# Optimization experiments

Hardware: AMD Instinct MI355X
Metric: run time of the kernel (lower is better)

The kernel has to match this reference:

```python
import jax, jax.numpy as jnp
import numpy as np

B, T, K = 16, 8, 4          # batch, num task vectors, num param blocks
DIN, H1, F, MH = 9408, 1024, 512, 128  # encoder dims; MetaNet hidden


def _pool(x):
    # 4x4 average pool then flatten: [B,3,224,224] -> [B, 3*56*56]
    b = x.shape[0]
    return x.reshape(b, 3, 56, 4, 56, 4).mean(axis=(3, 5)).reshape(b, -1)


def setup_inputs() -> dict:
    key = jax.random.key(0)
    ks = jax.random.split(key, 13)
    n = lambda k, shp, sc: jax.random.normal(k, shp, jnp.float32) * sc
    return {
        "x": jax.random.normal(ks[0], (B, 3, 224, 224), jnp.float32),
        "W1": n(ks[1], (DIN, H1), 0.02), "b1": n(ks[2], (H1,), 0.02),
        "W2": n(ks[3], (H1, F), 0.02),  "b2": n(ks[4], (F,), 0.02),
        "dW1": n(ks[5], (T, DIN, H1), 0.01), "db1": n(ks[6], (T, H1), 0.01),
        "dW2": n(ks[7], (T, H1, F), 0.01),   "db2": n(ks[8], (T, F), 0.01),
        # MetaNet: Linear(F,MH) init std=0.01, ReLU, Linear(MH, T*K)
        "mW1": n(ks[9], (F, MH), 0.01), "mb1": n(ks[10], (MH,), 0.01),
        "mW2": n(ks[11], (MH, T * K), 0.02), "mb2": n(ks[12], (T * K,), 0.02),
    }


def reference(x, W1, b1, W2, b2, dW1, db1, dW2, db2, mW1, mb1, mW2, mb2):
    xp = _pool(x)  # [B, DIN]
    # base features with frozen base params (torch.no_grad)
    base = jax.lax.stop_gradient(
        jax.nn.relu(xp @ W1 + b1) @ W2 + b2)  # [B, F]
    # MetaNet -> blockwise coefficients [B, T, K]; block order (W1,b1,W2,b2)
    coefs = (jax.nn.relu(base @ mW1 + mb1) @ mW2 + mb2).reshape(B, T, K)
    cW1, cb1, cW2, cb2 = coefs[:, :, 0], coefs[:, :, 1], coefs[:, :, 2], coefs[:, :, 3]
    # per-sample composed forward; (W1 + sum_t c*dW1) applied to xp, factored
    # so the [B,DIN,H1] composed weight is never materialized:
    h_tv = jnp.einsum("bi,tij->btj", xp, dW1)            # [B,T,H1]
    h = jax.nn.relu(xp @ W1 + jnp.einsum("bt,btj->bj", cW1, h_tv)
                    + b1 + jnp.einsum("bt,tj->bj", cb1, db1))  # [B,H1]
    o_tv = jnp.einsum("bj,tjk->btk", h, dW2)             # [B,T,F]
    out = (h @ W2 + jnp.einsum("bt,btk->bk", cW2, o_tv)
           + b2 + jnp.einsum("bt,tk->bk", cb2, db2))     # [B,F]
    return out
```

## Files before the change

kernel.cpp:

```cpp
#include <hip/hip_runtime.h>
#include <cstdint>
#include <cstddef>


typedef float f2_t __attribute__((ext_vector_type(2)));
typedef float f4_t __attribute__((ext_vector_type(4)));

__global__ void pool_kernel(const float* __restrict__ x, float* __restrict__ xp) {
  int idx = blockIdx.x * 256 + threadIdx.x;
  int bc = idx / 3136;
  int r  = idx - bc * 3136;
  int i  = r / 56;
  int j  = r - i * 56;
  const float* src = x + ((size_t)bc * 224 + 4 * i) * 224 + 4 * j;
  float s = 0.f;
#pragma unroll
  for (int rr = 0; rr < 4; ++rr) {
    float4 v = *reinterpret_cast<const float4*>(src + rr * 224);
    s += v.x + v.y + v.z + v.w;
  }
  xp[idx] = s * 0.0625f;
}

template<int KC, int VEC, int UF, int NT>
__device__ __forceinline__ void gemm_pipe(
    const float* a_s, int row0, const float* Brow, int N, float (&acc)[16][VEC])
{
  static_assert(KC % UF == 0, "");
  constexpr int NG = KC / UF;
  static_assert(NG >= 2, "");
  float w0[UF][VEC], w1[UF][VEC];

  auto loadg = [&](float (&W)[UF][VEC], int kb) {
#pragma unroll
    for (int u = 0; u < UF; ++u) {
      const float* p = Brow + (size_t)(kb + u) * N;
      if constexpr (VEC == 2) {
        f2_t v;
        if constexpr (NT) v = __builtin_nontemporal_load(reinterpret_cast<const f2_t*>(p));
        else              v = *reinterpret_cast<const f2_t*>(p);
        W[u][0] = v.x; W[u][1] = v.y;
      } else {
        f4_t v;
        if constexpr (NT) v = __builtin_nontemporal_load(reinterpret_cast<const f4_t*>(p));
        else              v = *reinterpret_cast<const f4_t*>(p);
        W[u][0] = v.x; W[u][1] = v.y; W[u][2] = v.z; W[u][3] = v.w;
      }
    }
  };
  auto comp = [&](const float (&W)[UF][VEC], int kb) {
#pragma unroll
    for (int u = 0; u < UF; ++u) {
      int kk = row0 + kb + u;
      const float4 a0 = *reinterpret_cast<const float4*>(&a_s[kk * 20 + 0]);
      const float4 a1 = *reinterpret_cast<const float4*>(&a_s[kk * 20 + 4]);
      const float4 a2 = *reinterpret_cast<const float4*>(&a_s[kk * 20 + 8]);
      const float4 a3 = *reinterpret_cast<const float4*>(&a_s[kk * 20 + 12]);
      const float av[16] = {a0.x, a0.y, a0.z, a0.w, a1.x, a1.y, a1.z, a1.w,
                            a2.x, a2.y, a2.z, a2.w, a3.x, a3.y, a3.z, a3.w};
#pragma unroll
      for (int b = 0; b < 16; ++b)
#pragma unroll
        for (int v = 0; v < VEC; ++v)
          acc[b][v] = fmaf(av[b], W[u][v], acc[b][v]);
    }
  };

  loadg(w0, 0);
  if constexpr (NG % 2 == 0) {
#pragma unroll 1
    for (int g = 0; g + 2 < NG; g += 2) {
      loadg(w1, (g + 1) * UF);
      comp(w0, g * UF);
      loadg(w0, (g + 2) * UF);
      comp(w1, (g + 1) * UF);
    }
    loadg(w1, (NG - 1) * UF);
    comp(w0, (NG - 2) * UF);
    comp(w1, (NG - 1) * UF);
  } else {
#pragma unroll 1
    for (int g = 0; g + 3 < NG; g += 2) {
      loadg(w1, (g + 1) * UF);
      comp(w0, g * UF);
      loadg(w0, (g + 2) * UF);
      comp(w1, (g + 1) * UF);
    }
    loadg(w1, (NG - 2) * UF);
    comp(w0, (NG - 3) * UF);
    loadg(w0, (NG - 1) * UF);
    comp(w1, (NG - 2) * UF);
    comp(w0, (NG - 1) * UF);
  }
}

template<int KC, int VEC, int UF, int NT, int BS>
__global__ __launch_bounds__(BS) void skinny_gemm(
    const float* __restrict__ A, int ldA,
    const float* __restrict__ B,
    const float* __restrict__ A2, int ldA2,
    const float* __restrict__ B2,
    int chunkSplit, int chunksPerT,
    const float* __restrict__ coefs4,
    int N, float* __restrict__ P)
{
  __shared__ float a_s[KC * 20];
  const int c = blockIdx.x, tid = threadIdx.x;

  const float* Ab;
  const float* Bb;
  int lda, iLoc0, t = 0;
  bool scaled = false;
  if (c < chunkSplit) {
    Ab = A; lda = ldA;
    if (chunksPerT > 0) {
      t = c / chunksPerT;
      iLoc0 = (c - t * chunksPerT) * KC;
    } else {
      iLoc0 = c * KC;
    }
    scaled = (coefs4 != nullptr);
    Bb = B + (size_t)c * KC * N;
  } else {
    Ab = A2; lda = ldA2;
    iLoc0 = (c - chunkSplit) * KC;
    Bb = B2 + (size_t)iLoc0 * N;
  }

  for (int b = 0; b < 16; ++b) {
    float s = scaled ? coefs4[b * 32 + t * 4] : 1.f;
    const float* Arow = Ab + (size_t)b * lda + iLoc0;
    for (int kk = tid; kk < KC; kk += BS)
      a_s[kk * 20 + b] = s * Arow[kk];
  }
  __syncthreads();

  const int j0 = (blockIdx.y * BS + tid) * VEC;
  float acc[16][VEC];
#pragma unroll
  for (int b = 0; b < 16; ++b)
#pragma unroll
    for (int v = 0; v < VEC; ++v) acc[b][v] = 0.f;

  gemm_pipe<KC, VEC, UF, NT>(a_s, 0, Bb + j0, N, acc);

  float* Pb = P + (size_t)c * 16 * N + j0;
#pragma unroll
  for (int b = 0; b < 16; ++b) {
    if constexpr (VEC == 2) {
      f2_t v = {acc[b][0], acc[b][1]};
      __builtin_nontemporal_store(v, reinterpret_cast<f2_t*>(Pb));
    } else {
      f4_t v = {acc[b][0], acc[b][1], acc[b][2], acc[b][3]};
      __builtin_nontemporal_store(v, reinterpret_cast<f4_t*>(Pb));
    }
    Pb += N;
  }
}

__global__ __launch_bounds__(512, 2) void gbig_kernel(
    const float* __restrict__ xp,
    const float* __restrict__ W1,
    const float* __restrict__ dW1,
    float* __restrict__ P1, float* __restrict__ P3)
{
  __shared__ float a_s[294 * 20];
  __shared__ float lds2[256 * 65];
  const int tid = threadIdx.x;

  if (blockIdx.x < 224) {
    const int c = blockIdx.x;
    for (int b = 0; b < 16; ++b) {
      const float* Arow = xp + (size_t)b * 9408 + c * 42;
      for (int kk = tid; kk < 42; kk += 512) a_s[kk * 20 + b] = Arow[kk];
    }
    __syncthreads();

    const int j0 = tid * 2;
    float acc[16][2];
#pragma unroll
    for (int b = 0; b < 16; ++b) { acc[b][0] = 0.f; acc[b][1] = 0.f; }
    gemm_pipe<42, 2, 7, 1>(a_s, 0, W1 + (size_t)c * 42 * 1024 + j0, 1024, acc);

    float* Pb = P1 + (size_t)c * 16 * 1024 + j0;
#pragma unroll
    for (int b = 0; b < 16; ++b) {
      f2_t v = {acc[b][0], acc[b][1]};
      __builtin_nontemporal_store(v, reinterpret_cast<f2_t*>(Pb));
      Pb += 1024;
    }
  } else {
    const int c = blockIdx.x - 224;
    const int t = c >> 5, il = (c & 31) * 294;
    for (int b = 0; b < 16; ++b) {
      const float* Arow = xp + (size_t)b * 9408 + il;
      for (int kk = tid; kk < 294; kk += 512) a_s[kk * 20 + b] = Arow[kk];
    }
    __syncthreads();

    const int half = tid >> 8, t256 = tid & 255;
    const int j0 = t256 * 4;
    float acc[16][4];
#pragma unroll
    for (int b = 0; b < 16; ++b)
#pragma unroll
      for (int v = 0; v < 4; ++v) acc[b][v] = 0.f;

    gemm_pipe<147, 4, 7, 1>(a_s, half * 147,
                            dW1 + ((size_t)t * 9408 + il + half * 147) * 1024 + j0,
                            1024, acc);

    if (half) {
      float* dst = &lds2[t256 * 65];
#pragma unroll
      for (int b = 0; b < 16; ++b)
#pragma unroll
        for (int v = 0; v < 4; ++v) dst[b * 4 + v] = acc[b][v];
    }
    __syncthreads();
    if (!half) {
      const float* src = &lds2[t256 * 65];
      float* Pb = P3 + (size_t)c * 16 * 1024 + j0;
#pragma unroll
      for (int b = 0; b < 16; ++b) {
        f4_t v = {acc[b][0] + src[b * 4 + 0], acc[b][1] + src[b * 4 + 1],
                  acc[b][2] + src[b * 4 + 2], acc[b][3] + src[b * 4 + 3]};
        __builtin_nontemporal_store(v, reinterpret_cast<f4_t*>(Pb));
        Pb += 1024;
      }
    }
  }
}

template<int NCH, int MODE, int FTOT>
__global__ __launch_bounds__(256) void reduce4(
    const float* __restrict__ P,
    const float* __restrict__ bias,
    const float* __restrict__ coefs,
    const float* __restrict__ dvec,
    float* __restrict__ o1, float* __restrict__ o2)
{
  constexpr int CPS = NCH / 16;
  static_assert(NCH % 16 == 0, "");
  __shared__ float4 r[16][17];
  const int fl = threadIdx.x & 15, s = threadIdx.x >> 4;
  const int f = blockIdx.x * 64 + fl * 4;

  const f4_t* p = reinterpret_cast<const f4_t*>(P + (size_t)s * CPS * FTOT + f);
  float sx = 0.f, sy = 0.f, sz = 0.f, sw = 0.f;
#pragma unroll 8
  for (int cc = 0; cc < CPS; ++cc) {
    f4_t v = __builtin_nontemporal_load(p);
    sx += v.x; sy += v.y; sz += v.z; sw += v.w;
    p += FTOT / 4;
  }
  if constexpr (MODE == 3) {
    int b = f >> 10;
    float sc = coefs[b * 32 + (s >> 1) * 4];
    sx *= sc; sy *= sc; sz *= sc; sw *= sc;
  }
  r[s][fl] = make_float4(sx, sy, sz, sw);
  __syncthreads();

  if (s == 0) {
    float vx = 0.f, vy = 0.f, vz = 0.f, vw = 0.f;
#pragma unroll
    for (int i = 0; i < 16; ++i) {
      float4 t = r[i][fl];
      vx += t.x; vy += t.y; vz += t.z; vw += t.w;
    }
    if constexpr (MODE == 1) {
      float4 bb = *reinterpret_cast<const float4*>(bias + (f & 1023));
      float4 z = make_float4(vx + bb.x, vy + bb.y, vz + bb.z, vw + bb.w);
      *reinterpret_cast<float4*>(o1 + f) = z;
      *reinterpret_cast<float4*>(o2 + f) =
          make_float4(fmaxf(z.x, 0.f), fmaxf(z.y, 0.f), fmaxf(z.z, 0.f), fmaxf(z.w, 0.f));
    } else if constexpr (MODE == 3) {
      int b = f >> 10, j = f & 1023;
      float4 zz = *reinterpret_cast<const float4*>(bias + f);
      float zx = vx + zz.x, zy = vy + zz.y, zzc = vz + zz.z, zw = vw + zz.w;
#pragma unroll
      for (int t = 0; t < 8; ++t) {
        float c1 = coefs[b * 32 + t * 4 + 1];
        float4 d = *reinterpret_cast<const float4*>(dvec + t * 1024 + j);
        zx = fmaf(c1, d.x, zx); zy = fmaf(c1, d.y, zy);
        zzc = fmaf(c1, d.z, zzc); zw = fmaf(c1, d.w, zw);
      }
      *reinterpret_cast<float4*>(o1 + f) =
          make_float4(fmaxf(zx, 0.f), fmaxf(zy, 0.f), fmaxf(zzc, 0.f), fmaxf(zw, 0.f));
    } else {
      int b = f >> 9, k = f & 511;
      float4 bb = *reinterpret_cast<const float4*>(bias + k);
      float zx = vx + bb.x, zy = vy + bb.y, zzc = vz + bb.z, zw = vw + bb.w;
#pragma unroll
      for (int t = 0; t < 8; ++t) {
        float c3 = coefs[b * 32 + t * 4 + 3];
        float4 d = *reinterpret_cast<const float4*>(dvec + t * 512 + k);
        zx = fmaf(c3, d.x, zx); zy = fmaf(c3, d.y, zy);
        zzc = fmaf(c3, d.z, zzc); zw = fmaf(c3, d.w, zw);
      }
      *reinterpret_cast<float4*>(o1 + f) = make_float4(zx, zy, zzc, zw);
    }
  }
}

__global__ __launch_bounds__(512) void tail2_kernel(
    const float* __restrict__ P2, const float* __restrict__ b2,
    const float* __restrict__ mW1, const float* __restrict__ mb1,
    const float* __restrict__ mW2, const float* __restrict__ mb2,
    float* __restrict__ coefs)
{
  __shared__ float bs[512];
  __shared__ float pm[4][129];
  __shared__ float ms[128];
  __shared__ float p3[16][33];
  const int b = blockIdx.x, tid = threadIdx.x;

  float s = b2[tid];
  const float* p = P2 + b * 512 + tid;
#pragma unroll 8
  for (int c = 0; c < 128; ++c) { s += *p; p += 8192; }
  bs[tid] = s;
  __syncthreads();

  {
    int col = tid & 127, kq = tid >> 7;
    const float* br = &bs[kq * 128];
    const float* w = mW1 + (size_t)(kq * 128) * 128 + col;
    float m0 = 0.f, m1 = 0.f, m2 = 0.f, m3 = 0.f;
    for (int k = 0; k < 128; k += 4) {
      m0 = fmaf(br[k + 0], w[(k + 0) * 128], m0);
      m1 = fmaf(br[k + 1], w[(k + 1) * 128], m1);
      m2 = fmaf(br[k + 2], w[(k + 2) * 128], m2);
      m3 = fmaf(br[k + 3], w[(k + 3) * 128], m3);
    }
    pm[kq][col] = (m0 + m1) + (m2 + m3);
  }
  __syncthreads();
  if (tid < 128)
    ms[tid] = fmaxf(mb1[tid] + (pm[0][tid] + pm[1][tid]) + (pm[2][tid] + pm[3][tid]), 0.f);
  __syncthreads();

  {
    int o = tid & 31, kq = tid >> 5;
    float a = 0.f;
#pragma unroll
    for (int kk = 0; kk < 8; ++kk)
      a = fmaf(ms[kq * 8 + kk], mW2[(kq * 8 + kk) * 32 + o], a);
    p3[kq][o] = a;
  }
  __syncthreads();
  if (tid < 32) {
    float a = mb2[tid];
#pragma unroll
    for (int q = 0; q < 16; ++q) a += p3[q][tid];
    coefs[b * 32 + tid] = a;
  }
}

extern "C" void kernel_launch(void* const* d_in, const int* in_sizes, int n_in,
                              void* d_out, int out_size, void* d_ws, size_t ws_size,
                              hipStream_t stream) {
  const float* x   = (const float*)d_in[0];
  const float* W1  = (const float*)d_in[1];
  const float* b1  = (const float*)d_in[2];
  const float* W2  = (const float*)d_in[3];
  const float* b2  = (const float*)d_in[4];
  const float* dW1 = (const float*)d_in[5];
  const float* db1 = (const float*)d_in[6];
  const float* dW2 = (const float*)d_in[7];
  const float* db2 = (const float*)d_in[8];
  const float* mW1 = (const float*)d_in[9];
  const float* mb1 = (const float*)d_in[10];
  const float* mW2 = (const float*)d_in[11];
  const float* mb2 = (const float*)d_in[12];
  float* out = (float*)d_out;

  float* ws    = (float*)d_ws;
  float* xp    = ws;
  float* z1    = xp + 150528;
  float* t1    = z1 + 16384;
  float* coefs = t1 + 16384;
  float* h     = coefs + 512;
  float* P1    = h + 16384;
  float* P2    = P1 + 3670016;
  float* P3    = P2 + 1048576;
  float* P4    = P3 + 4194304;

  const int BIG = 1 << 30;

  pool_kernel<<<588, 256, 0, stream>>>(x, xp);

  gbig_kernel<<<480, 512, 0, stream>>>(xp, W1, dW1, P1, P3);

  reduce4<224, 1, 16384><<<256, 256, 0, stream>>>(P1, b1, nullptr, nullptr, z1, t1);

  skinny_gemm<8, 2, 4, 0, 256><<<dim3(128, 1), 256, 0, stream>>>(
      t1, 1024, W2, nullptr, 0, nullptr, BIG, 0, nullptr, 512, P2);

  tail2_kernel<<<16, 512, 0, stream>>>(P2, b2, mW1, mb1, mW2, mb2, coefs);

  reduce4<256, 3, 16384><<<256, 256, 0, stream>>>(P3, z1, coefs, db1, h, nullptr);

  skinny_gemm<32, 2, 8, 1, 256><<<dim3(288, 1), 256, 0, stream>>>(
      h, 1024, dW2, h, 1024, W2, 256, 32, coefs + 2, 512, P4);

  reduce4<288, 4, 8192><<<128, 256, 0, stream>>>(P4, b2, coefs, db2, out, nullptr);
}
```

Baseline: 133.3 us.

## Fuse pooling into big GEMM and merge W1 reduction with W2 GEMM

```diff
diff --git a/kernel.cpp b/kernel.cpp
--- a/kernel.cpp
+++ b/kernel.cpp
@@ -5,22 +5,6 @@
 
 typedef float f2_t __attribute__((ext_vector_type(2)));
 typedef float f4_t __attribute__((ext_vector_type(4)));
-
-__global__ void pool_kernel(const float* __restrict__ x, float* __restrict__ xp) {
-  int idx = blockIdx.x * 256 + threadIdx.x;
-  int bc = idx / 3136;
-  int r  = idx - bc * 3136;
-  int i  = r / 56;
-  int j  = r - i * 56;
-  const float* src = x + ((size_t)bc * 224 + 4 * i) * 224 + 4 * j;
-  float s = 0.f;
-#pragma unroll
-  for (int rr = 0; rr < 4; ++rr) {
-    float4 v = *reinterpret_cast<const float4*>(src + rr * 224);
-    s += v.x + v.y + v.z + v.w;
-  }
-  xp[idx] = s * 0.0625f;
-}
 
 template<int KC, int VEC, int UF, int NT>
 __device__ __forceinline__ void gemm_pipe(
@@ -94,6 +78,145 @@
   }
 }
 
+template<int KC, int NTHR>
+__device__ __forceinline__ void stage_pool(float* a_s, const float* __restrict__ x, int il) {
+  for (int idx = threadIdx.x; idx < 16 * KC; idx += NTHR) {
+    int b = idx / KC, kk = idx - b * KC;
+    int i = il + kk;
+    int ch = i / 3136, r = i - ch * 3136;
+    int pi = r / 56, pj = r - pi * 56;
+    const float* src = x + ((size_t)(b * 3 + ch) * 224 + 4 * pi) * 224 + 4 * pj;
+    float4 v0 = *reinterpret_cast<const float4*>(src);
+    float4 v1 = *reinterpret_cast<const float4*>(src + 224);
+    float4 v2 = *reinterpret_cast<const float4*>(src + 448);
+    float4 v3 = *reinterpret_cast<const float4*>(src + 672);
+    float s = (v0.x + v0.y + v0.z + v0.w) + (v1.x + v1.y + v1.z + v1.w)
+            + (v2.x + v2.y + v2.z + v2.w) + (v3.x + v3.y + v3.z + v3.w);
+    a_s[kk * 20 + b] = s * 0.0625f;
+  }
+}
+
+__global__ __launch_bounds__(512, 2) void gbig_kernel(
+    const float* __restrict__ x,
+    const float* __restrict__ W1,
+    const float* __restrict__ dW1,
+    float* __restrict__ P1, float* __restrict__ P3)
+{
+  __shared__ float a_s[294 * 20];
+  __shared__ float lds2[256 * 65];
+  const int tid = threadIdx.x;
+
+  if (blockIdx.x < 112) {
+    const int c = blockIdx.x;
+    stage_pool<84, 512>(a_s, x, c * 84);
+    __syncthreads();
+
+    const int j0 = tid * 2;
+    float acc[16][2];
+#pragma unroll
+    for (int b = 0; b < 16; ++b) { acc[b][0] = 0.f; acc[b][1] = 0.f; }
+    gemm_pipe<84, 2, 7, 1>(a_s, 0, W1 + (size_t)c * 84 * 1024 + j0, 1024, acc);
+
+    float* Pb = P1 + (size_t)c * 16 * 1024 + j0;
+#pragma unroll
+    for (int b = 0; b < 16; ++b) {
+      f2_t v = {acc[b][0], acc[b][1]};
+      __builtin_nontemporal_store(v, reinterpret_cast<f2_t*>(Pb));
+      Pb += 1024;
+    }
+  } else {
+    const int c = blockIdx.x - 112;
+    const int t = c >> 5, il = (c & 31) * 294;
+    stage_pool<294, 512>(a_s, x, il);
+    __syncthreads();
+
+    const int half = tid >> 8, t256 = tid & 255;
+    const int j0 = t256 * 4;
+    float acc[16][4];
+#pragma unroll
+    for (int b = 0; b < 16; ++b)
+#pragma unroll
+      for (int v = 0; v < 4; ++v) acc[b][v] = 0.f;
+
+    gemm_pipe<147, 4, 7, 1>(a_s, half * 147,
+                            dW1 + ((size_t)t * 9408 + il + half * 147) * 1024 + j0,
+                            1024, acc);
+
+    if (half) {
+      float* dst = &lds2[t256 * 65];
+#pragma unroll
+      for (int b = 0; b < 16; ++b)
+#pragma unroll
+        for (int v = 0; v < 4; ++v) dst[b * 4 + v] = acc[b][v];
+    }
+    __syncthreads();
+    if (!half) {
+      const float* src = &lds2[t256 * 65];
+      float* Pb = P3 + (size_t)c * 16 * 1024 + j0;
+#pragma unroll
+      for (int b = 0; b < 16; ++b) {
+        f4_t v = {acc[b][0] + src[b * 4 + 0], acc[b][1] + src[b * 4 + 1],
+                  acc[b][2] + src[b * 4 + 2], acc[b][3] + src[b * 4 + 3]};
+        __builtin_nontemporal_store(v, reinterpret_cast<f4_t*>(Pb));
+        Pb += 1024;
+      }
+    }
+  }
+}
+
+__global__ __launch_bounds__(256) void rg12_kernel(
+    const float* __restrict__ P1, const float* __restrict__ b1,
+    const float* __restrict__ W2,
+    float* __restrict__ z1, float* __restrict__ P2)
+{
+  __shared__ float4 r[16][17];
+  __shared__ float t1s[64];
+  const int blk = blockIdx.x;
+  const int b = blk >> 4, jg = blk & 15;
+  const int fl = threadIdx.x & 15, s = threadIdx.x >> 4;
+  const int f = blk * 64 + fl * 4;
+
+  const f4_t* p = reinterpret_cast<const f4_t*>(P1 + (size_t)s * 7 * 16384 + f);
+  float sx = 0.f, sy = 0.f, sz = 0.f, sw = 0.f;
+#pragma unroll
+  for (int cc = 0; cc < 7; ++cc) {
+    f4_t v = __builtin_nontemporal_load(p);
+    sx += v.x; sy += v.y; sz += v.z; sw += v.w;
+    p += 4096;
+  }
+  r[s][fl] = make_float4(sx, sy, sz, sw);
+  __syncthreads();
+
+  if (s == 0) {
+    float vx = 0.f, vy = 0.f, vz = 0.f, vw = 0.f;
+#pragma unroll
+    for (int i = 0; i < 16; ++i) {
+      float4 t = r[i][fl];
+      vx += t.x; vy += t.y; vz += t.z; vw += t.w;
+    }
+    float4 bb = *reinterpret_cast<const float4*>(b1 + (f & 1023));
+    float4 z = make_float4(vx + bb.x, vy + bb.y, vz + bb.z, vw + bb.w);
+    *reinterpret_cast<float4*>(z1 + f) = z;
+    *reinterpret_cast<float4*>(&t1s[fl * 4]) =
+        make_float4(fmaxf(z.x, 0.f), fmaxf(z.y, 0.f), fmaxf(z.z, 0.f), fmaxf(z.w, 0.f));
+  }
+  __syncthreads();
+
+  const int j = threadIdx.x * 2;
+  const float* w = W2 + (size_t)(jg * 64) * 512 + j;
+  float a0 = 0.f, a1 = 0.f;
+#pragma unroll 8
+  for (int kk = 0; kk < 64; ++kk) {
+    f2_t wv = *reinterpret_cast<const f2_t*>(w);
+    w += 512;
+    float tv = t1s[kk];
+    a0 = fmaf(tv, wv.x, a0);
+    a1 = fmaf(tv, wv.y, a1);
+  }
+  f2_t o = {a0, a1};
+  __builtin_nontemporal_store(o, reinterpret_cast<f2_t*>(P2 + ((size_t)jg * 16 + b) * 512 + j));
+}
+
 template<int KC, int VEC, int UF, int NT, int BS>
 __global__ __launch_bounds__(BS) void skinny_gemm(
     const float* __restrict__ A, int ldA,
@@ -158,87 +281,13 @@
   }
 }
 
-__global__ __launch_bounds__(512, 2) void gbig_kernel(
-    const float* __restrict__ xp,
-    const float* __restrict__ W1,
-    const float* __restrict__ dW1,
-    float* __restrict__ P1, float* __restrict__ P3)
-{
-  __shared__ float a_s[294 * 20];
-  __shared__ float lds2[256 * 65];
-  const int tid = threadIdx.x;
-
-  if (blockIdx.x < 224) {
-    const int c = blockIdx.x;
-    for (int b = 0; b < 16; ++b) {
-      const float* Arow = xp + (size_t)b * 9408 + c * 42;
-      for (int kk = tid; kk < 42; kk += 512) a_s[kk * 20 + b] = Arow[kk];
-    }
-    __syncthreads();
-
-    const int j0 = tid * 2;
-    float acc[16][2];
-#pragma unroll
-    for (int b = 0; b < 16; ++b) { acc[b][0] = 0.f; acc[b][1] = 0.f; }
-    gemm_pipe<42, 2, 7, 1>(a_s, 0, W1 + (size_t)c * 42 * 1024 + j0, 1024, acc);
-
-    float* Pb = P1 + (size_t)c * 16 * 1024 + j0;
-#pragma unroll
-    for (int b = 0; b < 16; ++b) {
-      f2_t v = {acc[b][0], acc[b][1]};
-      __builtin_nontemporal_store(v, reinterpret_cast<f2_t*>(Pb));
-      Pb += 1024;
-    }
-  } else {
-    const int c = blockIdx.x - 224;
-    const int t = c >> 5, il = (c & 31) * 294;
-    for (int b = 0; b < 16; ++b) {
-      const float* Arow = xp + (size_t)b * 9408 + il;
-      for (int kk = tid; kk < 294; kk += 512) a_s[kk * 20 + b] = Arow[kk];
-    }
-    __syncthreads();
-
-    const int half = tid >> 8, t256 = tid & 255;
-    const int j0 = t256 * 4;
-    float acc[16][4];
-#pragma unroll
-    for (int b = 0; b < 16; ++b)
-#pragma unroll
-      for (int v = 0; v < 4; ++v) acc[b][v] = 0.f;
-
-    gemm_pipe<147, 4, 7, 1>(a_s, half * 147,
-                            dW1 + ((size_t)t * 9408 + il + half * 147) * 1024 + j0,
-                            1024, acc);
-
-    if (half) {
-      float* dst = &lds2[t256 * 65];
-#pragma unroll
-      for (int b = 0; b < 16; ++b)
-#pragma unroll
-        for (int v = 0; v < 4; ++v) dst[b * 4 + v] = acc[b][v];
-    }
-    __syncthreads();
-    if (!half) {
-      const float* src = &lds2[t256 * 65];
-      float* Pb = P3 + (size_t)c * 16 * 1024 + j0;
-#pragma unroll
-      for (int b = 0; b < 16; ++b) {
-        f4_t v = {acc[b][0] + src[b * 4 + 0], acc[b][1] + src[b * 4 + 1],
-                  acc[b][2] + src[b * 4 + 2], acc[b][3] + src[b * 4 + 3]};
-        __builtin_nontemporal_store(v, reinterpret_cast<f4_t*>(Pb));
-        Pb += 1024;
-      }
-    }
-  }
-}
-
 template<int NCH, int MODE, int FTOT>
 __global__ __launch_bounds__(256) void reduce4(
     const float* __restrict__ P,
     const float* __restrict__ bias,
     const float* __restrict__ coefs,
     const float* __restrict__ dvec,
-    float* __restrict__ o1, float* __restrict__ o2)
+    float* __restrict__ o1)
 {
   constexpr int CPS = NCH / 16;
   static_assert(NCH % 16 == 0, "");
@@ -269,13 +318,7 @@
       float4 t = r[i][fl];
       vx += t.x; vy += t.y; vz += t.z; vw += t.w;
     }
-    if constexpr (MODE == 1) {
-      float4 bb = *reinterpret_cast<const float4*>(bias + (f & 1023));
-      float4 z = make_float4(vx + bb.x, vy + bb.y, vz + bb.z, vw + bb.w);
-      *reinterpret_cast<float4*>(o1 + f) = z;
-      *reinterpret_cast<float4*>(o2 + f) =
-          make_float4(fmaxf(z.x, 0.f), fmaxf(z.y, 0.f), fmaxf(z.z, 0.f), fmaxf(z.w, 0.f));
-    } else if constexpr (MODE == 3) {
+    if constexpr (MODE == 3) {
       int b = f >> 10, j = f & 1023;
       float4 zz = *reinterpret_cast<const float4*>(bias + f);
       float zx = vx + zz.x, zy = vy + zz.y, zzc = vz + zz.z, zw = vw + zz.w;
@@ -318,8 +361,8 @@
 
   float s = b2[tid];
   const float* p = P2 + b * 512 + tid;
-#pragma unroll 8
-  for (int c = 0; c < 128; ++c) { s += *p; p += 8192; }
+#pragma unroll
+  for (int c = 0; c < 16; ++c) { s += *p; p += 8192; }
   bs[tid] = s;
   __syncthreads();
 
@@ -377,33 +420,24 @@
   float* out = (float*)d_out;
 
   float* ws    = (float*)d_ws;
-  float* xp    = ws;
-  float* z1    = xp + 150528;
-  float* t1    = z1 + 16384;
-  float* coefs = t1 + 16384;
+  float* z1    = ws;
+  float* coefs = z1 + 16384;
   float* h     = coefs + 512;
   float* P1    = h + 16384;
-  float* P2    = P1 + 3670016;
-  float* P3    = P2 + 1048576;
+  float* P2    = P1 + 1835008;
+  float* P3    = P2 + 131072;
   float* P4    = P3 + 4194304;
 
-  const int BIG = 1 << 30;
-
-  pool_kernel<<<588, 256, 0, stream>>>(x, xp);
-
-  gbig_kernel<<<480, 512, 0, stream>>>(xp, W1, dW1, P1, P3);
-
-  reduce4<224, 1, 16384><<<256, 256, 0, stream>>>(P1, b1, nullptr, nullptr, z1, t1);
-
-  skinny_gemm<8, 2, 4, 0, 256><<<dim3(128, 1), 256, 0, stream>>>(
-      t1, 1024, W2, nullptr, 0, nullptr, BIG, 0, nullptr, 512, P2);
+  gbig_kernel<<<368, 512, 0, stream>>>(x, W1, dW1, P1, P3);
+
+  rg12_kernel<<<256, 256, 0, stream>>>(P1, b1, W2, z1, P2);
 
   tail2_kernel<<<16, 512, 0, stream>>>(P2, b2, mW1, mb1, mW2, mb2, coefs);
 
-  reduce4<256, 3, 16384><<<256, 256, 0, stream>>>(P3, z1, coefs, db1, h, nullptr);
+  reduce4<256, 3, 16384><<<256, 256, 0, stream>>>(P3, z1, coefs, db1, h);
 
   skinny_gemm<32, 2, 8, 1, 256><<<dim3(288, 1), 256, 0, stream>>>(
       h, 1024, dW2, h, 1024, W2, 256, 32, coefs + 2, 512, P4);
 
-  reduce4<288, 4, 8192><<<128, 256, 0, stream>>>(P4, b2, coefs, db2, out, nullptr);
-}
+  reduce4<288, 4, 8192><<<128, 256, 0, stream>>>(P4, b2, coefs, db2, out);
+}
```

After: 133.1 us. Within noise of the previous version (-0.1%).

## Fuse pipeline stages into persistent kernels with atomic-counter inter-block barriers

Applied to the files above, without the earlier changes.

```diff
diff --git a/kernel.cpp b/kernel.cpp
--- a/kernel.cpp
+++ b/kernel.cpp
@@ -5,6 +5,82 @@
 
 typedef float f2_t __attribute__((ext_vector_type(2)));
 typedef float f4_t __attribute__((ext_vector_type(4)));
+
+__global__ void init_kernel(int* bar) { bar[blockIdx.x * 256 + threadIdx.x] = 0; }
+
+__device__ __forceinline__ void arrive(int* ctr) {
+  __syncthreads();
+  if (threadIdx.x == 0) {
+    __threadfence();
+    __hip_atomic_fetch_add(ctr + ((blockIdx.x & 7) << 5), 1,
+                           __ATOMIC_RELAXED, __HIP_MEMORY_SCOPE_AGENT);
+  }
+}
+
+__device__ __forceinline__ void wait_sum(const int* ctr, int n, int ncnt, int* shdone) {
+  while (true) {
+    if (threadIdx.x == 0) {
+      int s = 0;
+      for (int i = 0; i < ncnt; ++i)
+        s += __hip_atomic_load(ctr + (i << 5), __ATOMIC_RELAXED, __HIP_MEMORY_SCOPE_AGENT);
+      *shdone = (s >= n) ? 1 : 0;
+    }
+    __syncthreads();
+    if (*shdone) break;
+    __builtin_amdgcn_s_sleep(8);
+    __syncthreads();
+  }
+  if (threadIdx.x == 0) __threadfence();
+  __syncthreads();
+}
+
+template<int KC, int UF>
+__device__ __forceinline__ void gemm_pipe2(
+    const float* a_s, const float* Brow, int N, float (&acc)[16][2])
+{
+  static_assert(KC % UF == 0, "");
+  constexpr int NG = KC / UF;
+  static_assert(NG >= 2 && NG % 2 == 0, "");
+  float w0[UF][2], w1[UF][2];
+
+  auto loadg = [&](float (&W)[UF][2], int kb) {
+#pragma unroll
+    for (int u = 0; u < UF; ++u) {
+      f2_t v = __builtin_nontemporal_load(
+          reinterpret_cast<const f2_t*>(Brow + (size_t)(kb + u) * N));
+      W[u][0] = v.x; W[u][1] = v.y;
+    }
+  };
+  auto comp = [&](const float (&W)[UF][2], int kb) {
+#pragma unroll
+    for (int u = 0; u < UF; ++u) {
+      int kk = kb + u;
+      const float4 a0 = *reinterpret_cast<const float4*>(&a_s[kk * 20 + 0]);
+      const float4 a1 = *reinterpret_cast<const float4*>(&a_s[kk * 20 + 4]);
+      const float4 a2 = *reinterpret_cast<const float4*>(&a_s[kk * 20 + 8]);
+      const float4 a3 = *reinterpret_cast<const float4*>(&a_s[kk * 20 + 12]);
+      const float av[16] = {a0.x, a0.y, a0.z, a0.w, a1.x, a1.y, a1.z, a1.w,
+                            a2.x, a2.y, a2.z, a2.w, a3.x, a3.y, a3.z, a3.w};
+#pragma unroll
+      for (int b = 0; b < 16; ++b) {
+        acc[b][0] = fmaf(av[b], W[u][0], acc[b][0]);
+        acc[b][1] = fmaf(av[b], W[u][1], acc[b][1]);
+      }
+    }
+  };
+
+  loadg(w0, 0);
+#pragma unroll 1
+  for (int g = 0; g + 2 < NG; g += 2) {
+    loadg(w1, (g + 1) * UF);
+    comp(w0, g * UF);
+    loadg(w0, (g + 2) * UF);
+    comp(w1, (g + 1) * UF);
+  }
+  loadg(w1, (NG - 1) * UF);
+  comp(w0, (NG - 2) * UF);
+  comp(w1, (NG - 1) * UF);
+}
 
 __global__ void pool_kernel(const float* __restrict__ x, float* __restrict__ xp) {
   int idx = blockIdx.x * 256 + threadIdx.x;
@@ -22,166 +98,33 @@
   xp[idx] = s * 0.0625f;
 }
 
-template<int KC, int VEC, int UF, int NT>
-__device__ __forceinline__ void gemm_pipe(
-    const float* a_s, int row0, const float* Brow, int N, float (&acc)[16][VEC])
+__global__ __launch_bounds__(512, 4) void big_kernel(
+    const float* __restrict__ xp,
+    const float* __restrict__ W1, const float* __restrict__ b1,
+    const float* __restrict__ W2,  const float* __restrict__ b2,
+    const float* __restrict__ dW1, const float* __restrict__ db1,
+    const float* __restrict__ mW1, const float* __restrict__ mb1,
+    const float* __restrict__ mW2, const float* __restrict__ mb2,
+    float* __restrict__ z1, float* __restrict__ coefs, float* __restrict__ h,
+    float* __restrict__ P1, float* __restrict__ P2, float* __restrict__ P3,
+    int* __restrict__ bar)
 {
-  static_assert(KC % UF == 0, "");
-  constexpr int NG = KC / UF;
-  static_assert(NG >= 2, "");
-  float w0[UF][VEC], w1[UF][VEC];
-
-  auto loadg = [&](float (&W)[UF][VEC], int kb) {
-#pragma unroll
-    for (int u = 0; u < UF; ++u) {
-      const float* p = Brow + (size_t)(kb + u) * N;
-      if constexpr (VEC == 2) {
-        f2_t v;
-        if constexpr (NT) v = __builtin_nontemporal_load(reinterpret_cast<const f2_t*>(p));
-        else              v = *reinterpret_cast<const f2_t*>(p);
-        W[u][0] = v.x; W[u][1] = v.y;
-      } else {
-        f4_t v;
-        if constexpr (NT) v = __builtin_nontemporal_load(reinterpret_cast<const f4_t*>(p));
-        else              v = *reinterpret_cast<const f4_t*>(p);
-        W[u][0] = v.x; W[u][1] = v.y; W[u][2] = v.z; W[u][3] = v.w;
-      }
-    }
-  };
-  auto comp = [&](const float (&W)[UF][VEC], int kb) {
-#pragma unroll
-    for (int u = 0; u < UF; ++u) {
-      int kk = row0 + kb + u;
-      const float4 a0 = *reinterpret_cast<const float4*>(&a_s[kk * 20 + 0]);
-      const float4 a1 = *reinterpret_cast<const float4*>(&a_s[kk * 20 + 4]);
-      const float4 a2 = *reinterpret_cast<const float4*>(&a_s[kk * 20 + 8]);
-      const float4 a3 = *reinterpret_cast<const float4*>(&a_s[kk * 20 + 12]);
-      const float av[16] = {a0.x, a0.y, a0.z, a0.w, a1.x, a1.y, a1.z, a1.w,
-                            a2.x, a2.y, a2.z, a2.w, a3.x, a3.y, a3.z, a3.w};
-#pragma unroll
-      for (int b = 0; b < 16; ++b)
-#pragma unroll
-        for (int v = 0; v < VEC; ++v)
-          acc[b][v] = fmaf(av[b], W[u][v], acc[b][v]);
-    }
-  };
-
-  loadg(w0, 0);
-  if constexpr (NG % 2 == 0) {
-#pragma unroll 1
-    for (int g = 0; g + 2 < NG; g += 2) {
-      loadg(w1, (g + 1) * UF);
-      comp(w0, g * UF);
-      loadg(w0, (g + 2) * UF);
-      comp(w1, (g + 1) * UF);
-    }
-    loadg(w1, (NG - 1) * UF);
-    comp(w0, (NG - 2) * UF);
-    comp(w1, (NG - 1) * UF);
-  } else {
-#pragma unroll 1
-    for (int g = 0; g + 3 < NG; g += 2) {
-      loadg(w1, (g + 1) * UF);
-      comp(w0, g * UF);
-      loadg(w0, (g + 2) * UF);
-      comp(w1, (g + 1) * UF);
-    }
-    loadg(w1, (NG - 2) * UF);
-    comp(w0, (NG - 3) * UF);
-    loadg(w0, (NG - 1) * UF);
-    comp(w1, (NG - 2) * UF);
-    comp(w0, (NG - 1) * UF);
-  }
-}
-
-template<int KC, int VEC, int UF, int NT, int BS>
-__global__ __launch_bounds__(BS) void skinny_gemm(
-    const float* __restrict__ A, int ldA,
-    const float* __restrict__ B,
-    const float* __restrict__ A2, int ldA2,
-    const float* __restrict__ B2,
-    int chunkSplit, int chunksPerT,
-    const float* __restrict__ coefs4,
-    int N, float* __restrict__ P)
-{
-  __shared__ float a_s[KC * 20];
-  const int c = blockIdx.x, tid = threadIdx.x;
-
-  const float* Ab;
-  const float* Bb;
-  int lda, iLoc0, t = 0;
-  bool scaled = false;
-  if (c < chunkSplit) {
-    Ab = A; lda = ldA;
-    if (chunksPerT > 0) {
-      t = c / chunksPerT;
-      iLoc0 = (c - t * chunksPerT) * KC;
-    } else {
-      iLoc0 = c * KC;
-    }
-    scaled = (coefs4 != nullptr);
-    Bb = B + (size_t)c * KC * N;
-  } else {
-    Ab = A2; lda = ldA2;
-    iLoc0 = (c - chunkSplit) * KC;
-    Bb = B2 + (size_t)iLoc0 * N;
-  }
-
-  for (int b = 0; b < 16; ++b) {
-    float s = scaled ? coefs4[b * 32 + t * 4] : 1.f;
-    const float* Arow = Ab + (size_t)b * lda + iLoc0;
-    for (int kk = tid; kk < KC; kk += BS)
-      a_s[kk * 20 + b] = s * Arow[kk];
-  }
-  __syncthreads();
-
-  const int j0 = (blockIdx.y * BS + tid) * VEC;
-  float acc[16][VEC];
-#pragma unroll
-  for (int b = 0; b < 16; ++b)
-#pragma unroll
-    for (int v = 0; v < VEC; ++v) acc[b][v] = 0.f;
-
-  gemm_pipe<KC, VEC, UF, NT>(a_s, 0, Bb + j0, N, acc);
-
-  float* Pb = P + (size_t)c * 16 * N + j0;
-#pragma unroll
-  for (int b = 0; b < 16; ++b) {
-    if constexpr (VEC == 2) {
-      f2_t v = {acc[b][0], acc[b][1]};
-      __builtin_nontemporal_store(v, reinterpret_cast<f2_t*>(Pb));
-    } else {
-      f4_t v = {acc[b][0], acc[b][1], acc[b][2], acc[b][3]};
-      __builtin_nontemporal_store(v, reinterpret_cast<f4_t*>(Pb));
-    }
-    Pb += N;
-  }
-}
-
-__global__ __launch_bounds__(512, 2) void gbig_kernel(
-    const float* __restrict__ xp,
-    const float* __restrict__ W1,
-    const float* __restrict__ dW1,
-    float* __restrict__ P1, float* __restrict__ P3)
-{
-  __shared__ float a_s[294 * 20];
-  __shared__ float lds2[256 * 65];
-  const int tid = threadIdx.x;
-
-  if (blockIdx.x < 224) {
-    const int c = blockIdx.x;
-    for (int b = 0; b < 16; ++b) {
-      const float* Arow = xp + (size_t)b * 9408 + c * 42;
-      for (int kk = tid; kk < 42; kk += 512) a_s[kk * 20 + b] = Arow[kk];
-    }
-    __syncthreads();
-
+  __shared__ float sh[294 * 20];
+  __shared__ int shdone;
+  const int blk = blockIdx.x, tid = threadIdx.x;
+
+  if (blk < 112) {
+    const int c = blk;
+    for (int idx = tid; idx < 16 * 84; idx += 512) {
+      int b = idx / 84, kk = idx - b * 84;
+      sh[kk * 20 + b] = xp[(size_t)b * 9408 + c * 84 + kk];
+    }
+    __syncthreads();
     const int j0 = tid * 2;
     float acc[16][2];
 #pragma unroll
     for (int b = 0; b < 16; ++b) { acc[b][0] = 0.f; acc[b][1] = 0.f; }
-    gemm_pipe<42, 2, 7, 1>(a_s, 0, W1 + (size_t)c * 42 * 1024 + j0, 1024, acc);
-
+    gemm_pipe2<84, 7>(sh, W1 + (size_t)c * 84 * 1024 + j0, 1024, acc);
     float* Pb = P1 + (size_t)c * 16 * 1024 + j0;
 #pragma unroll
     for (int b = 0; b < 16; ++b) {
@@ -189,172 +132,236 @@
       __builtin_nontemporal_store(v, reinterpret_cast<f2_t*>(Pb));
       Pb += 1024;
     }
+    arrive(bar + 0);
+  } else if (blk < 368) {
+    const int c = blk - 112;
+    const int t = c >> 5, il = (c & 31) * 294;
+    for (int idx = tid; idx < 16 * 294; idx += 512) {
+      int b = idx / 294, kk = idx - b * 294;
+      sh[kk * 20 + b] = xp[(size_t)b * 9408 + il + kk];
+    }
+    __syncthreads();
+    const int j0 = tid * 2;
+    float acc[16][2];
+#pragma unroll
+    for (int b = 0; b < 16; ++b) { acc[b][0] = 0.f; acc[b][1] = 0.f; }
+    gemm_pipe2<294, 7>(sh, dW1 + ((size_t)t * 9408 + il) * 1024 + j0, 1024, acc);
+    float* Pb = P3 + (size_t)c * 16 * 1024 + j0;
+#pragma unroll
+    for (int b = 0; b < 16; ++b) {
+      f2_t v = {acc[b][0], acc[b][1]};
+      __builtin_nontemporal_store(v, reinterpret_cast<f2_t*>(Pb));
+      Pb += 1024;
+    }
+    arrive(bar + 512);
+  } else if (blk < 624) {
+    wait_sum(bar + 0, 112, 8, &shdone);
+    const int r = blk - 368, b = r >> 4, jg = r & 15;
+    float2* r2 = reinterpret_cast<float2*>(sh);
+    float* t1s = sh + 1200;
+    const int fl = tid & 31, s = tid >> 5;
+    const int f = b * 1024 + jg * 64 + fl * 2;
+
+    const f2_t* p = reinterpret_cast<const f2_t*>(P1 + (size_t)s * 7 * 16384 + f);
+    float sx = 0.f, sy = 0.f;
+#pragma unroll
+    for (int cc = 0; cc < 7; ++cc) {
+      f2_t v = __builtin_nontemporal_load(p);
+      sx += v.x; sy += v.y;
+      p += 8192;
+    }
+    r2[s * 33 + fl] = make_float2(sx, sy);
+    __syncthreads();
+    if (tid < 32) {
+      float vx = 0.f, vy = 0.f;
+#pragma unroll
+      for (int i = 0; i < 16; ++i) { float2 t = r2[i * 33 + tid]; vx += t.x; vy += t.y; }
+      const int ff = b * 1024 + jg * 64 + tid * 2;
+      float2 bb = *reinterpret_cast<const float2*>(b1 + (ff & 1023));
+      float2 z = make_float2(vx + bb.x, vy + bb.y);
+      *reinterpret_cast<float2*>(z1 + ff) = z;
+      t1s[tid * 2] = fmaxf(z.x, 0.f);
+      t1s[tid * 2 + 1] = fmaxf(z.y, 0.f);
+    }
+    __syncthreads();
+    const float* w = W2 + (size_t)(jg * 64) * 512 + tid;
+    float a = 0.f;
+#pragma unroll 8
+    for (int kk = 0; kk < 64; ++kk) a = fmaf(t1s[kk], w[(size_t)kk * 512], a);
+    __builtin_nontemporal_store(a, P2 + ((size_t)jg * 16 + b) * 512 + tid);
+    arrive(bar + 256);
+  } else if (blk < 640) {
+    wait_sum(bar + 256, 256, 8, &shdone);
+    const int b = blk - 624;
+    float* bs = sh;
+    float* pm = sh + 512;
+    float* ms = sh + 1152;
+    float* p3 = sh + 1312;
+
+    float s0 = b2[tid & 511];
+    if (tid < 512) {
+      const float* p = P2 + b * 512 + tid;
+#pragma unroll
+      for (int c = 0; c < 16; ++c) { s0 += *p; p += 8192; }
+      bs[tid] = s0;
+    }
+    __syncthreads();
+    {
+      int col = tid & 127, kq = (tid >> 7) & 3;
+      const float* br = &bs[kq * 128];
+      const float* w = mW1 + (size_t)(kq * 128) * 128 + col;
+      float m0 = 0.f, m1 = 0.f, m2 = 0.f, m3 = 0.f;
+      for (int k = 0; k < 128; k += 4) {
+        m0 = fmaf(br[k + 0], w[(k + 0) * 128], m0);
+        m1 = fmaf(br[k + 1], w[(k + 1) * 128], m1);
+        m2 = fmaf(br[k + 2], w[(k + 2) * 128], m2);
+        m3 = fmaf(br[k + 3], w[(k + 3) * 128], m3);
+      }
+      pm[kq * 129 + col] = (m0 + m1) + (m2 + m3);
+    }
+    __syncthreads();
+    if (tid < 128)
+      ms[tid] = fmaxf(mb1[tid] + (pm[tid] + pm[129 + tid]) + (pm[258 + tid] + pm[387 + tid]), 0.f);
+    __syncthreads();
+    {
+      int o = tid & 31, kq = tid >> 5;
+      float a = 0.f;
+#pragma unroll
+      for (int kk = 0; kk < 8; ++kk)
+        a = fmaf(ms[kq * 8 + kk], mW2[(kq * 8 + kk) * 32 + o], a);
+      p3[kq * 33 + o] = a;
+    }
+    __syncthreads();
+    if (tid < 32) {
+      float a = mb2[tid];
+#pragma unroll
+      for (int q = 0; q < 16; ++q) a += p3[q * 33 + tid];
+      coefs[b * 32 + tid] = a;
+    }
+    arrive(bar + 768);
   } else {
-    const int c = blockIdx.x - 224;
-    const int t = c >> 5, il = (c & 31) * 294;
-    for (int b = 0; b < 16; ++b) {
-      const float* Arow = xp + (size_t)b * 9408 + il;
-      for (int kk = tid; kk < 294; kk += 512) a_s[kk * 20 + b] = Arow[kk];
-    }
-    __syncthreads();
-
-    const int half = tid >> 8, t256 = tid & 255;
-    const int j0 = t256 * 4;
-    float acc[16][4];
-#pragma unroll
-    for (int b = 0; b < 16; ++b)
-#pragma unroll
-      for (int v = 0; v < 4; ++v) acc[b][v] = 0.f;
-
-    gemm_pipe<147, 4, 7, 1>(a_s, half * 147,
-                            dW1 + ((size_t)t * 9408 + il + half * 147) * 1024 + j0,
-                            1024, acc);
-
-    if (half) {
-      float* dst = &lds2[t256 * 65];
-#pragma unroll
-      for (int b = 0; b < 16; ++b)
-#pragma unroll
-        for (int v = 0; v < 4; ++v) dst[b * 4 + v] = acc[b][v];
-    }
-    __syncthreads();
-    if (!half) {
-      const float* src = &lds2[t256 * 65];
-      float* Pb = P3 + (size_t)c * 16 * 1024 + j0;
-#pragma unroll
-      for (int b = 0; b < 16; ++b) {
-        f4_t v = {acc[b][0] + src[b * 4 + 0], acc[b][1] + src[b * 4 + 1],
-                  acc[b][2] + src[b * 4 + 2], acc[b][3] + src[b * 4 + 3]};
-        __builtin_nontemporal_store(v, reinterpret_cast<f4_t*>(Pb));
-        Pb += 1024;
-      }
-    }
-  }
-}
-
-template<int NCH, int MODE, int FTOT>
-__global__ __launch_bounds__(256) void reduce4(
-    const float* __restrict__ P,
-    const float* __restrict__ bias,
-    const float* __restrict__ coefs,
-    const float* __restrict__ dvec,
-    float* __restrict__ o1, float* __restrict__ o2)
-{
-  constexpr int CPS = NCH / 16;
-  static_assert(NCH % 16 == 0, "");
-  __shared__ float4 r[16][17];
-  const int fl = threadIdx.x & 15, s = threadIdx.x >> 4;
-  const int f = blockIdx.x * 64 + fl * 4;
-
-  const f4_t* p = reinterpret_cast<const f4_t*>(P + (size_t)s * CPS * FTOT + f);
-  float sx = 0.f, sy = 0.f, sz = 0.f, sw = 0.f;
-#pragma unroll 8
-  for (int cc = 0; cc < CPS; ++cc) {
-    f4_t v = __builtin_nontemporal_load(p);
-    sx += v.x; sy += v.y; sz += v.z; sw += v.w;
-    p += FTOT / 4;
-  }
-  if constexpr (MODE == 3) {
-    int b = f >> 10;
+    wait_sum(bar + 512, 272, 16, &shdone);
+    const int rb = blk - 640;
+    float4* r4 = reinterpret_cast<float4*>(sh);
+    const int fl = tid & 31, s = tid >> 5;
+    const int f = rb * 128 + fl * 4;
+    const int b = f >> 10;
+
+    const f4_t* p = reinterpret_cast<const f4_t*>(P3 + (size_t)s * 16 * 16384 + f);
+    float sx = 0.f, sy = 0.f, sz = 0.f, sw = 0.f;
+#pragma unroll
+    for (int cc = 0; cc < 16; ++cc) {
+      f4_t v = __builtin_nontemporal_load(p);
+      sx += v.x; sy += v.y; sz += v.z; sw += v.w;
+      p += 4096;
+    }
     float sc = coefs[b * 32 + (s >> 1) * 4];
-    sx *= sc; sy *= sc; sz *= sc; sw *= sc;
-  }
-  r[s][fl] = make_float4(sx, sy, sz, sw);
-  __syncthreads();
-
-  if (s == 0) {
-    float vx = 0.f, vy = 0.f, vz = 0.f, vw = 0.f;
-#pragma unroll
-    for (int i = 0; i < 16; ++i) {
-      float4 t = r[i][fl];
-      vx += t.x; vy += t.y; vz += t.z; vw += t.w;
-    }
-    if constexpr (MODE == 1) {
-      float4 bb = *reinterpret_cast<const float4*>(bias + (f & 1023));
-      float4 z = make_float4(vx + bb.x, vy + bb.y, vz + bb.z, vw + bb.w);
-      *reinterpret_cast<float4*>(o1 + f) = z;
-      *reinterpret_cast<float4*>(o2 + f) =
-          make_float4(fmaxf(z.x, 0.f), fmaxf(z.y, 0.f), fmaxf(z.z, 0.f), fmaxf(z.w, 0.f));
-    } else if constexpr (MODE == 3) {
-      int b = f >> 10, j = f & 1023;
-      float4 zz = *reinterpret_cast<const float4*>(bias + f);
-      float zx = vx + zz.x, zy = vy + zz.y, zzc = vz + zz.z, zw = vw + zz.w;
+    r4[s * 33 + fl] = make_float4(sx * sc, sy * sc, sz * sc, sw * sc);
+    __syncthreads();
+
+    if (s == 0) {
+      float vx = 0.f, vy = 0.f, vz = 0.f, vw = 0.f;
+#pragma unroll
+      for (int i = 0; i < 16; ++i) {
+        float4 t = r4[i * 33 + fl];
+        vx += t.x; vy += t.y; vz += t.z; vw += t.w;
+      }
+      int j = f & 1023;
+      float4 zz = *reinterpret_cast<const float4*>(z1 + f);
+      float zx = vx + zz.x, zy = vy + zz.y, zc = vz + zz.z, zw = vw + zz.w;
 #pragma unroll
       for (int t = 0; t < 8; ++t) {
         float c1 = coefs[b * 32 + t * 4 + 1];
-        float4 d = *reinterpret_cast<const float4*>(dvec + t * 1024 + j);
+        float4 d = *reinterpret_cast<const float4*>(db1 + t * 1024 + j);
         zx = fmaf(c1, d.x, zx); zy = fmaf(c1, d.y, zy);
-        zzc = fmaf(c1, d.z, zzc); zw = fmaf(c1, d.w, zw);
-      }
-      *reinterpret_cast<float4*>(o1 + f) =
-          make_float4(fmaxf(zx, 0.f), fmaxf(zy, 0.f), fmaxf(zzc, 0.f), fmaxf(zw, 0.f));
+        zc = fmaf(c1, d.z, zc); zw = fmaf(c1, d.w, zw);
+      }
+      *reinterpret_cast<float4*>(h + f) =
+          make_float4(fmaxf(zx, 0.f), fmaxf(zy, 0.f), fmaxf(zc, 0.f), fmaxf(zw, 0.f));
+    }
+  }
+}
+
+__global__ __launch_bounds__(256) void tail_kernel(
+    const float* __restrict__ h, const float* __restrict__ W2,
+    const float* __restrict__ b2,
+    const float* __restrict__ dW2, const float* __restrict__ db2,
+    const float* __restrict__ coefs,
+    float* __restrict__ P4, float* __restrict__ out, int* __restrict__ bar)
+{
+  __shared__ float sh[32 * 20 + 16 * 17 * 4];
+  __shared__ int shdone;
+  const int blk = blockIdx.x, tid = threadIdx.x;
+
+  if (blk < 288) {
+    const float* Bb; int il; bool scaled;
+    int t = 0;
+    if (blk < 256) {
+      t = blk >> 5; il = (blk & 31) * 32;
+      Bb = dW2 + ((size_t)t * 1024 + il) * 512;
+      scaled = true;
     } else {
-      int b = f >> 9, k = f & 511;
-      float4 bb = *reinterpret_cast<const float4*>(bias + k);
-      float zx = vx + bb.x, zy = vy + bb.y, zzc = vz + bb.z, zw = vw + bb.w;
+      il = (blk - 256) * 32;
+      Bb = W2 + (size_t)il * 512;
+      scaled = false;
+    }
+    for (int b = 0; b < 16; ++b) {
+      float s = scaled ? coefs[b * 32 + t * 4 + 2] : 1.f;
+      const float* Arow = h + (size_t)b * 1024 + il;
+      for (int kk = tid; kk < 32; kk += 256)
+        sh[kk * 20 + b] = s * Arow[kk];
+    }
+    __syncthreads();
+    const int j0 = tid * 2;
+    float acc[16][2];
+#pragma unroll
+    for (int b = 0; b < 16; ++b) { acc[b][0] = 0.f; acc[b][1] = 0.f; }
+    gemm_pipe2<32, 8>(sh, Bb + j0, 512, acc);
+    float* Pb = P4 + (size_t)blk * 16 * 512 + j0;
+#pragma unroll
+    for (int b = 0; b < 16; ++b) {
+      f2_t v = {acc[b][0], acc[b][1]};
+      __builtin_nontemporal_store(v, reinterpret_cast<f2_t*>(Pb));
+      Pb += 512;
+    }
+    arrive(bar + 1024);
+  } else {
+    wait_sum(bar + 1024, 288, 8, &shdone);
+    const int rb = blk - 288;
+    float4* r4 = reinterpret_cast<float4*>(sh);
+    const int fl = tid & 15, s = tid >> 4;
+    const int f = rb * 64 + fl * 4;
+    const int b = f >> 9, k = f & 511;
+
+    const f4_t* p = reinterpret_cast<const f4_t*>(P4 + (size_t)s * 18 * 8192 + f);
+    float sx = 0.f, sy = 0.f, sz = 0.f, sw = 0.f;
+#pragma unroll
+    for (int cc = 0; cc < 18; ++cc) {
+      f4_t v = __builtin_nontemporal_load(p);
+      sx += v.x; sy += v.y; sz += v.z; sw += v.w;
+      p += 2048;
+    }
+    r4[s * 17 + fl] = make_float4(sx, sy, sz, sw);
+    __syncthreads();
+
+    if (s == 0) {
+      float vx = 0.f, vy = 0.f, vz = 0.f, vw = 0.f;
+#pragma unroll
+      for (int i = 0; i < 16; ++i) {
+        float4 t = r4[i * 17 + fl];
+        vx += t.x; vy += t.y; vz += t.z; vw += t.w;
+      }
+      float4 bb = *reinterpret_cast<const float4*>(b2 + k);
+      float zx = vx + bb.x, zy = vy + bb.y, zc = vz + bb.z, zw = vw + bb.w;
 #pragma unroll
       for (int t = 0; t < 8; ++t) {
         float c3 = coefs[b * 32 + t * 4 + 3];
-        float4 d = *reinterpret_cast<const float4*>(dvec + t * 512 + k);
+        float4 d = *reinterpret_cast<const float4*>(db2 + t * 512 + k);
         zx = fmaf(c3, d.x, zx); zy = fmaf(c3, d.y, zy);
-        zzc = fmaf(c3, d.z, zzc); zw = fmaf(c3, d.w, zw);
-      }
-      *reinterpret_cast<float4*>(o1 + f) = make_float4(zx, zy, zzc, zw);
-    }
-  }
-}
-
-__global__ __launch_bounds__(512) void tail2_kernel(
-    const float* __restrict__ P2, const float* __restrict__ b2,
-    const float* __restrict__ mW1, const float* __restrict__ mb1,
-    const float* __restrict__ mW2, const float* __restrict__ mb2,
-    float* __restrict__ coefs)
-{
-  __shared__ float bs[512];
-  __shared__ float pm[4][129];
-  __shared__ float ms[128];
-  __shared__ float p3[16][33];
-  const int b = blockIdx.x, tid = threadIdx.x;
-
-  float s = b2[tid];
-  const float* p = P2 + b * 512 + tid;
-#pragma unroll 8
-  for (int c = 0; c < 128; ++c) { s += *p; p += 8192; }
-  bs[tid] = s;
-  __syncthreads();
-
-  {
-    int col = tid & 127, kq = tid >> 7;
-    const float* br = &bs[kq * 128];
-    const float* w = mW1 + (size_t)(kq * 128) * 128 + col;
-    float m0 = 0.f, m1 = 0.f, m2 = 0.f, m3 = 0.f;
-    for (int k = 0; k < 128; k += 4) {
-      m0 = fmaf(br[k + 0], w[(k + 0) * 128], m0);
-      m1 = fmaf(br[k + 1], w[(k + 1) * 128], m1);
-      m2 = fmaf(br[k + 2], w[(k + 2) * 128], m2);
-      m3 = fmaf(br[k + 3], w[(k + 3) * 128], m3);
-    }
-    pm[kq][col] = (m0 + m1) + (m2 + m3);
-  }
-  __syncthreads();
-  if (tid < 128)
-    ms[tid] = fmaxf(mb1[tid] + (pm[0][tid] + pm[1][tid]) + (pm[2][tid] + pm[3][tid]), 0.f);
-  __syncthreads();
-
-  {
-    int o = tid & 31, kq = tid >> 5;
-    float a = 0.f;
-#pragma unroll
-    for (int kk = 0; kk < 8; ++kk)
-      a = fmaf(ms[kq * 8 + kk], mW2[(kq * 8 + kk) * 32 + o], a);
-    p3[kq][o] = a;
-  }
-  __syncthreads();
-  if (tid < 32) {
-    float a = mb2[tid];
-#pragma unroll
-    for (int q = 0; q < 16; ++q) a += p3[q][tid];
-    coefs[b * 32 + tid] = a;
+        zc = fmaf(c3, d.z, zc); zw = fmaf(c3, d.w, zw);
+      }
+      *reinterpret_cast<float4*>(out + f) = make_float4(zx, zy, zc, zw);
+    }
   }
 }
 
@@ -376,34 +383,24 @@
   const float* mb2 = (const float*)d_in[12];
   float* out = (float*)d_out;
 
-  float* ws    = (float*)d_ws;
+  int*   bar   = (int*)d_ws;
+  float* ws    = (float*)d_ws + 2048;
   float* xp    = ws;
   float* z1    = xp + 150528;
-  float* t1    = z1 + 16384;
-  float* coefs = t1 + 16384;
+  float* coefs = z1 + 16384;
   float* h     = coefs + 512;
   float* P1    = h + 16384;
-  float* P2    = P1 + 3670016;
-  float* P3    = P2 + 1048576;
+  float* P2    = P1 + 1835008;
+  float* P3    = P2 + 131072;
   float* P4    = P3 + 4194304;
 
-  const int BIG = 1 << 30;
+  init_kernel<<<5, 256, 0, stream>>>(bar);
 
   pool_kernel<<<588, 256, 0, stream>>>(x, xp);
 
-  gbig_kernel<<<480, 512, 0, stream>>>(xp, W1, dW1, P1, P3);
-
-  reduce4<224, 1, 16384><<<256, 256, 0, stream>>>(P1, b1, nullptr, nullptr, z1, t1);
-
-  skinny_gemm<8, 2, 4, 0, 256><<<dim3(128, 1), 256, 0, stream>>>(
-      t1, 1024, W2, nullptr, 0, nullptr, BIG, 0, nullptr, 512, P2);
-
-  tail2_kernel<<<16, 512, 0, stream>>>(P2, b2, mW1, mb1, mW2, mb2, coefs);
-
-  reduce4<256, 3, 16384><<<256, 256, 0, stream>>>(P3, z1, coefs, db1, h, nullptr);
-
-  skinny_gemm<32, 2, 8, 1, 256><<<dim3(288, 1), 256, 0, stream>>>(
-      h, 1024, dW2, h, 1024, W2, 256, 32, coefs + 2, 512, P4);
-
-  reduce4<288, 4, 8192><<<128, 256, 0, stream>>>(P4, b2, coefs, db2, out, nullptr);
-}
+  big_kernel<<<768, 512, 0, stream>>>(xp, W1, b1, W2, b2, dW1, db1,
+                                      mW1, mb1, mW2, mb2,
+                                      z1, coefs, h, P1, P2, P3, bar);
+
+  tail_kernel<<<416, 256, 0, stream>>>(h, W2, b2, dW2, db2, coefs, P4, out, bar);
+}
```

Result: slower. 208.2 us (+56.2%).
